# Kernel tuning notes

Measured on AMD Instinct MI355X. Metric: run time of the kernel, lower is better.

## Reference

```python
import jax, jax.numpy as jnp
import numpy as np

N_DRUG, N_MICROBE = 1500, 1572
N = N_DRUG + N_MICROBE          # 3072 nodes
F_IN = 1546                     # raw feature dim (fc1: 1546 -> 256)
D0 = 256                        # GCN input dim after fc1
H1 = H2 = 128                   # GCN hidden dims (H1 + H2 = 256)
B = 16384                       # number of (left,right) query pairs


def _sym_norm(A):
    # D^{-1/2} A D^{-1/2} (no self loops), zeros kept for isolated nodes
    deg = A.sum(axis=1)
    d = jnp.where(deg > 0, jax.lax.rsqrt(deg), 0.0)
    return A * d[:, None] * d[None, :]


def _compute_inf(adj, L):
    # dl.compute_inf: L-hop influence = L-th power of sym-normalized adjacency
    An = _sym_norm(adj)
    M = An
    for _ in range(L - 1):
        M = M @ An
    return M


def _gcn_norm(W):
    # GCNConv normalization: add self loops (weight 1), sym-normalize by weighted degree
    Ahat = W + jnp.eye(W.shape[0], dtype=W.dtype)
    deg = Ahat.sum(axis=1)
    d = jnp.where(deg > 0, jax.lax.rsqrt(deg), 0.0)
    return Ahat * d[:, None] * d[None, :]


def _glorot(key, shape):
    return jax.random.normal(key, shape, dtype=jnp.float32) / np.sqrt(shape[0])


def setup_inputs() -> dict:
    key = jax.random.key(0)
    ks = jax.random.split(key, 24)
    u = jax.random.uniform(ks[0], (N, N), dtype=jnp.float32)
    w = jax.random.uniform(ks[1], (N, N), dtype=jnp.float32)
    adj = jnp.where(u < 0.01, w, 0.0)
    adj = jnp.maximum(adj, adj.T)
    X = jax.random.normal(ks[2], (N, F_IN), dtype=jnp.float32)
    left = jax.random.randint(ks[3], (B,), 0, N)
    right = jax.random.randint(ks[4], (B,), 0, N)
    return dict(
        left=left, right=right, X=X, adj=adj, threshold=jnp.float32(1e-4),
        W_fc1=_glorot(ks[5], (F_IN, D0)), b_fc1=jnp.zeros((D0,), jnp.float32),
        Wg1=_glorot(ks[6], (D0, H1)), bg1=jnp.zeros((H1,), jnp.float32),
        Wg2=_glorot(ks[7], (H1, H2)), bg2=jnp.zeros((H2,), jnp.float32),
        Wg3=_glorot(ks[8], (D0, H1)), bg3=jnp.zeros((H1,), jnp.float32),
        Wg4=_glorot(ks[9], (H1, H2)), bg4=jnp.zeros((H2,), jnp.float32),
        Wg5=_glorot(ks[10], (D0, H1)), bg5=jnp.zeros((H1,), jnp.float32),
        Wg6=_glorot(ks[11], (H1, H2)), bg6=jnp.zeros((H2,), jnp.float32),
        cnn_k=jax.random.normal(ks[12], (1, 3, 3, 3), dtype=jnp.float32) * 0.1,
        cnn_b=jnp.zeros((1,), jnp.float32),
        W_a=_glorot(ks[13], (2 * (H1 + H2), 64)), b_a=jnp.zeros((64,), jnp.float32),
        W_b=_glorot(ks[14], (64, 2)), b_b=jnp.zeros((2,), jnp.float32),
    )


def reference(left, right, X, adj, threshold,
              W_fc1, b_fc1, Wg1, bg1, Wg2, bg2, Wg3, bg3, Wg4, bg4,
              Wg5, bg5, Wg6, bg6, cnn_k, cnn_b, W_a, b_a, W_b, b_b):
    X0 = jax.nn.relu(X @ W_fc1 + b_fc1)  # fc1: [N, 1546] -> [N, 256]

    def branch(mask_src, Wa, ba, Wb, bb):
        # dynamically thresholded edges carry the ORIGINAL adj weights
        Wadj = jnp.where(mask_src > threshold, adj, 0.0)
        An = _gcn_norm(Wadj)                       # [N, N]
        e1 = jax.nn.relu(An @ (X0 @ Wa) + ba)      # GCNConv 1
        e2 = jax.nn.relu(An @ (e1 @ Wb) + bb)      # GCNConv 2
        return jnp.concatenate([e1, e2], axis=1)   # [N, 256]

    emb_l2 = branch(_compute_inf(adj, 2), Wg1, bg1, Wg2, bg2)
    emb_l1 = branch(_compute_inf(adj, 1), Wg3, bg3, Wg4, bg4)
    emb_l0 = branch(adj, Wg5, bg5, Wg6, bg6)

    emb = jnp.stack([emb_l0, emb_l1, emb_l2], axis=0)[None]  # [1, 3, N, 256]
    conv = jax.lax.conv_general_dilated(
        emb, cnn_k, window_strides=(1, 1), padding=[(2, 2), (2, 2)],
        rhs_dilation=(2, 2), dimension_numbers=('NCHW', 'OIHW', 'NCHW'))
    emb_all = conv[0, 0] + cnn_b[0]                # [N, 256]

    pair = jnp.concatenate([emb_all[left], emb_all[right]], axis=1)  # [B, 512]
    h = jax.nn.relu(pair @ W_a + b_a)              # dropout is identity at eval
    logits = h @ W_b + b_b                         # [B, 2]
    return logits, emb_all
```

## Files before the change

### kernel.cpp

```cpp
#include <hip/hip_runtime.h>

#define NN 3072
#define FIN 1546
#define KP 1568
#define MAXR 192

#define XS4_BLOCKS (NN * KP / 1024)
#define WSPLIT_BLOCKS (256 * KP / 256)
#define WGA_BLOCKS 384
#define CSR_BLOCKS (NN / 4)
#define FC1_BLOCKS (NN / 16 * 4)

typedef __attribute__((ext_vector_type(8))) __bf16 bf16x8;
typedef __attribute__((ext_vector_type(4))) __bf16 bf16x4;
typedef __attribute__((ext_vector_type(4))) float f32x4;

__global__ __launch_bounds__(256) void prep1_k(const float* __restrict__ X,
                                               __bf16* __restrict__ Xh, __bf16* __restrict__ Xl,
                                               const float* __restrict__ W,
                                               __bf16* __restrict__ WhT, __bf16* __restrict__ WlT,
                                               const float* __restrict__ Wga0,
                                               const float* __restrict__ Wga1,
                                               const float* __restrict__ Wga2,
                                               __bf16* __restrict__ WgaTh, __bf16* __restrict__ WgaTl) {
    int bid = blockIdx.x;
    if (bid < XS4_BLOCKS) {
        int e = (bid * 256 + threadIdx.x) * 4;
        int i = e / KP, c = e - i * KP;
        const float* xr = X + (size_t)i * FIN + c;
        float x0 = (c + 0 < FIN) ? xr[0] : 0.f;
        float x1 = (c + 1 < FIN) ? xr[1] : 0.f;
        float x2 = (c + 2 < FIN) ? xr[2] : 0.f;
        float x3 = (c + 3 < FIN) ? xr[3] : 0.f;
        __bf16 h0 = (__bf16)x0, h1 = (__bf16)x1, h2 = (__bf16)x2, h3 = (__bf16)x3;
        bf16x4 hv = {h0, h1, h2, h3};
        bf16x4 lv = {(__bf16)(x0 - (float)h0), (__bf16)(x1 - (float)h1),
                     (__bf16)(x2 - (float)h2), (__bf16)(x3 - (float)h3)};
        *(bf16x4*)(Xh + e) = hv;
        *(bf16x4*)(Xl + e) = lv;
        return;
    }
    bid -= XS4_BLOCKS;
    if (bid < WSPLIT_BLOCKS) {
        int idx = bid * 256 + threadIdx.x;
        int c = idx / KP, k = idx - c * KP;
        float x = (k < FIN) ? W[(size_t)k * 256 + c] : 0.f;
        __bf16 h = (__bf16)x;
        WhT[idx] = h;
        WlT[idx] = (__bf16)(x - (float)h);
        return;
    }
    bid -= WSPLIT_BLOCKS;
    int idx = bid * 256 + threadIdx.x;
    int b = idx >> 15, r = idx & 32767;
    int c = r >> 8, k = r & 255;
    const float* Wp = (b == 0) ? Wga0 : (b == 1) ? Wga1 : Wga2;
    float x = Wp[k * 128 + c];
    __bf16 h = (__bf16)x;
    WgaTh[idx] = h;
    WgaTl[idx] = (__bf16)(x - (float)h);
}

__global__ __launch_bounds__(256) void fc1csr_k(const float* __restrict__ adj,
                                                int* __restrict__ cols, float* __restrict__ vals,
                                                int* __restrict__ cnt, float* __restrict__ dvec,
                                                const __bf16* __restrict__ Xh,
                                                const __bf16* __restrict__ Xl,
                                                const __bf16* __restrict__ WhT,
                                                const __bf16* __restrict__ WlT,
                                                const float* __restrict__ bias,
                                                __bf16* __restrict__ X0h,
                                                __bf16* __restrict__ X0l) {
    int bid = blockIdx.x, tid = threadIdx.x;
    if (bid < FC1_BLOCKS) {
        int rt = bid >> 2;
        int c0 = (bid & 3) * 64;
        int w = tid >> 6, lane = tid & 63;
        int m = lane & 15, q = lane >> 4;
        int r0 = rt * 16;
        int cw = c0 + w * 16;
        const __bf16* xh = Xh + (size_t)(r0 + m) * KP + q * 8;
        const __bf16* xl = Xl + (size_t)(r0 + m) * KP + q * 8;
        const __bf16* bh = WhT + (size_t)(cw + m) * KP + q * 8;
        const __bf16* bl = WlT + (size_t)(cw + m) * KP + q * 8;

        f32x4 acc;
        #pragma unroll
        for (int r = 0; r < 4; r++) acc[r] = 0.f;

        #pragma unroll 7
        for (int ks = 0; ks < KP; ks += 32) {
            bf16x8 ah = *(const bf16x8*)(xh + ks);
            bf16x8 al = *(const bf16x8*)(xl + ks);
            bf16x8 bhv = *(const bf16x8*)(bh + ks);
            bf16x8 blv = *(const bf16x8*)(bl + ks);
            acc = __builtin_amdgcn_mfma_f32_16x16x32_bf16(ah, bhv, acc, 0, 0, 0);
            acc = __builtin_amdgcn_mfma_f32_16x16x32_bf16(ah, blv, acc, 0, 0, 0);
            acc = __builtin_amdgcn_mfma_f32_16x16x32_bf16(al, bhv, acc, 0, 0, 0);
        }
        int col = cw + m;
        float bv = bias[col];
        #pragma unroll
        for (int r = 0; r < 4; r++) {
            int row = r0 + q * 4 + r;
            float s = fmaxf(acc[r] + bv, 0.f);
            __bf16 h = (__bf16)s;
            X0h[(size_t)row * 256 + col] = h;
            X0l[(size_t)row * 256 + col] = (__bf16)(s - (float)h);
        }
        return;
    }
    int i = (bid - FC1_BLOCKS) * 4 + (tid >> 6);
    int lane = tid & 63;
    const float* row = adj + (size_t)i * NN;
    unsigned long long below = (1ull << lane) - 1ull;
    float s = 0.f; int count = 0;
    int base = i * MAXR;
    for (int c0 = 0; c0 < NN; c0 += 256) {
        float4 a4 = *(const float4*)(row + c0 + lane * 4);
        float a[4] = {a4.x, a4.y, a4.z, a4.w};
        s += a[0] + a[1] + a[2] + a[3];
        unsigned long long bal[4];
        #pragma unroll
        for (int u = 0; u < 4; u++) bal[u] = __ballot(a[u] != 0.f);
        int before = 0;
        #pragma unroll
        for (int u = 0; u < 4; u++) before += __popcll(bal[u] & below);
        int local = 0;
        #pragma unroll
        for (int u = 0; u < 4; u++) {
            if (a[u] != 0.f) {
                int pos = count + before + local;
                if (pos < MAXR) { cols[base + pos] = c0 + lane * 4 + u; vals[base + pos] = a[u]; }
                local++;
            }
        }
        int tot = 0;
        #pragma unroll
        for (int u = 0; u < 4; u++) tot += __popcll(bal[u]);
        count += tot;
    }
    for (int off = 32; off; off >>= 1) s += __shfl_xor(s, off);
    if (lane == 0) {
        cnt[i] = count < MAXR ? count : MAXR;
        dvec[i] = (s > 0.f) ? 1.0f / sqrtf(s) : 0.f;
    }
}

__global__ __launch_bounds__(256) void maskg1_k(const int* __restrict__ cols,
                                                const float* __restrict__ vals,
                                                const int* __restrict__ cnt,
                                                const float* __restrict__ dvec,
                                                const float* __restrict__ thrp,
                                                int* __restrict__ mcols,
                                                float* __restrict__ mvals,
                                                int* __restrict__ mcnt,
                                                float* __restrict__ db,
                                                const __bf16* __restrict__ X0h,
                                                const __bf16* __restrict__ X0l,
                                                const __bf16* __restrict__ WgaTh,
                                                const __bf16* __restrict__ WgaTl,
                                                float* __restrict__ XWall) {
    __shared__ float ds[NN];
    __shared__ int lcols[MAXR];
    __shared__ float lvals[MAXR];
    __shared__ int lcnt;
    __shared__ float osum;
    int bid = blockIdx.x, tid = threadIdx.x;

    if (bid >= 3 * NN) {
        int g = bid - 3 * NN;
        int bx = g % 48, by = (g / 48) & 1, bz = g / 96;
        int w = tid >> 6, lane = tid & 63;
        int m = lane & 15, q = lane >> 4;
        int i0 = bx * 64, c0 = by * 64;
        int rowA = i0 + w * 16 + m;
        const __bf16* ah = X0h + (size_t)rowA * 256 + q * 8;
        const __bf16* al = X0l + (size_t)rowA * 256 + q * 8;
        const __bf16* bh0 = WgaTh + (size_t)bz * 128 * 256 + (size_t)(c0 + m) * 256 + q * 8;
        const __bf16* bl0 = WgaTl + (size_t)bz * 128 * 256 + (size_t)(c0 + m) * 256 + q * 8;

        f32x4 acc[4];
        #pragma unroll
        for (int ct = 0; ct < 4; ct++)
            #pragma unroll
            for (int r = 0; r < 4; r++) acc[ct][r] = 0.f;

        for (int ks = 0; ks < 256; ks += 32) {
            bf16x8 a_h = *(const bf16x8*)(ah + ks);
            bf16x8 a_l = *(const bf16x8*)(al + ks);
            #pragma unroll
            for (int ct = 0; ct < 4; ct++) {
                bf16x8 b_h = *(const bf16x8*)(bh0 + (size_t)ct * 16 * 256 + ks);
                bf16x8 b_l = *(const bf16x8*)(bl0 + (size_t)ct * 16 * 256 + ks);
                acc[ct] = __builtin_amdgcn_mfma_f32_16x16x32_bf16(a_h, b_h, acc[ct], 0, 0, 0);
                acc[ct] = __builtin_amdgcn_mfma_f32_16x16x32_bf16(a_h, b_l, acc[ct], 0, 0, 0);
                acc[ct] = __builtin_amdgcn_mfma_f32_16x16x32_bf16(a_l, b_h, acc[ct], 0, 0, 0);
            }
        }
        float* outp = XWall + (size_t)bz * NN * 128;
        int rowBase = i0 + w * 16 + q * 4;
        #pragma unroll
        for (int ct = 0; ct < 4; ct++) {
            int col = c0 + ct * 16 + m;
            #pragma unroll
            for (int r = 0; r < 4; r++)
                outp[(size_t)(rowBase + r) * 128 + col] = acc[ct][r];
        }
        return;
    }

    int t = bid;
    int mode, i;
    if (t < NN)          { mode = 2; i = t; }
    else if (t < 2 * NN) { mode = 0; i = t - NN; }
    else                 { mode = 1; i = t - 2 * NN; }

    mcols += (size_t)mode * NN * MAXR;
    mvals += (size_t)mode * NN * MAXR;
    mcnt  += (size_t)mode * NN;
    db    += (size_t)mode * NN;
    int ni = cnt[i], base = i * MAXR;
    float thr = *thrp;
    float di = dvec[i];

    if (mode < 2) {
        if (tid == 0) lcnt = 0;
        __syncthreads();
        float s = 0.f;
        if (tid < ni) {
            int j = cols[base + tid];
            float a = vals[base + tid];
            float m = (mode == 0) ? a : a * di * dvec[j];
            if (m > thr) {
                int p = atomicAdd(&lcnt, 1);
                mcols[base + p] = j;
                mvals[base + p] = a;
                s = a;
            }
        }
        ds[tid] = s; __syncthreads();
        for (int off = 128; off; off >>= 1) {
            if (tid < off) ds[tid] += ds[tid + off];
            __syncthreads();
        }
        if (tid == 0) {
            mcnt[i] = lcnt;
            db[i] = 1.0f / sqrtf(ds[0] + 1.0f);
        }
        return;
    }

    if (tid == 0) { osum = 0.f; lcnt = 0; }
    for (int j = tid; j < NN; j += 256) ds[j] = 0.f;
    __syncthreads();
    for (int t2 = tid; t2 < ni; t2 += 256) {
        int j = cols[base + t2];
        float a = vals[base + t2];
        lcols[t2] = j; lvals[t2] = a;
        ds[j] = a * dvec[j] * dvec[j];
    }
    __syncthreads();
    int lane = tid & 63, wv = tid >> 6;
    int sub = lane & 7, dg = lane >> 3;
    for (int o = wv * 8 + dg; o < ni; o += 32) {
        int j = lcols[o];
        int nj = cnt[j], bj = j * MAXR;
        float dot = 0.f;
        for (int t2 = sub; t2 < nj; t2 += 8)
            dot += vals[bj + t2] * ds[cols[bj + t2]];
        #pragma unroll
        for (int off = 4; off; off >>= 1) dot += __shfl_xor(dot, off);
        if (sub == 0 && di * dvec[j] * dot > thr) {
            int p = atomicAdd(&lcnt, 1);
            mcols[base + p] = j;
            mvals[base + p] = lvals[o];
            atomicAdd(&osum, lvals[o]);
        }
    }
    __syncthreads();
    if (tid == 0) {
        mcnt[i] = lcnt;
        db[i] = 1.0f / sqrtf(osum + 1.0f);
    }
}

__global__ __launch_bounds__(256) void spmm3_k(const int* __restrict__ mcols,
                                               const float* __restrict__ mvals,
                                               const int* __restrict__ mcnt,
                                               const float* __restrict__ db,
                                               const float* __restrict__ Xin,
                                               const float* __restrict__ bias0,
                                               const float* __restrict__ bias1,
                                               const float* __restrict__ bias2,
                                               float* __restrict__ embf, int coff,
                                               const float* __restrict__ Wgb0,
                                               const float* __restrict__ Wgb1,
                                               const float* __restrict__ Wgb2,
                                               float* __restrict__ HW2out) {
    __shared__ float lcoef[MAXR];
    __shared__ int lj[MAXR];
    __shared__ float4 part[8][32];
    __shared__ float e1row[128];
    __shared__ float part2[2][128];
    int i = blockIdx.x, tid = threadIdx.x, b = blockIdx.y;
    mcols += (size_t)b * NN * MAXR;
    mvals += (size_t)b * NN * MAXR;
    mcnt  += (size_t)b * NN;
    db    += (size_t)b * NN;
    const float* Xb = Xin + (size_t)b * NN * 128;
    const float* bias = (b == 0) ? bias0 : (b == 1) ? bias1 : bias2;
    float dbi = db[i];
    int n = mcnt[i], base = i * MAXR;
    if (tid < n) {
        int j = mcols[base + tid];
        lj[tid] = j;
        lcoef[tid] = mvals[base + tid] * dbi * db[j];
    }
    __syncthreads();
    int g = tid >> 5, c4 = (tid & 31) << 2;
    float4 acc = make_float4(0.f, 0.f, 0.f, 0.f);
    float4 acc2 = make_float4(0.f, 0.f, 0.f, 0.f);
    if (g == 0) {
        float4 x = *(const float4*)&Xb[(size_t)i * 128 + c4];
        float d2 = dbi * dbi;
        acc = make_float4(d2 * x.x, d2 * x.y, d2 * x.z, d2 * x.w);
    }
    int t = g;
    for (; t + 8 < n; t += 16) {
        float cf0 = lcoef[t];
        float4 x0 = *(const float4*)&Xb[(size_t)lj[t] * 128 + c4];
        float cf1 = lcoef[t + 8];
        float4 x1 = *(const float4*)&Xb[(size_t)lj[t + 8] * 128 + c4];
        acc.x += cf0 * x0.x; acc.y += cf0 * x0.y; acc.z += cf0 * x0.z; acc.w += cf0 * x0.w;
        acc2.x += cf1 * x1.x; acc2.y += cf1 * x1.y; acc2.z += cf1 * x1.z; acc2.w += cf1 * x1.w;
    }
    if (t < n) {
        float cf = lcoef[t];
        float4 x = *(const float4*)&Xb[(size_t)lj[t] * 128 + c4];
        acc.x += cf * x.x; acc.y += cf * x.y; acc.z += cf * x.z; acc.w += cf * x.w;
    }
    acc.x += acc2.x; acc.y += acc2.y; acc.z += acc2.z; acc.w += acc2.w;
    part[g][tid & 31] = acc;
    __syncthreads();
    if (tid < 32) {
        float4 s = part[0][tid];
        #pragma unroll
        for (int gg = 1; gg < 8; gg++) {
            float4 t4 = part[gg][tid];
            s.x += t4.x; s.y += t4.y; s.z += t4.z; s.w += t4.w;
        }
        int cc = tid << 2;
        float4 bv = *(const float4*)&bias[cc];
        s.x = fmaxf(s.x + bv.x, 0.f); s.y = fmaxf(s.y + bv.y, 0.f);
        s.z = fmaxf(s.z + bv.z, 0.f); s.w = fmaxf(s.w + bv.w, 0.f);
        *(float4*)&embf[((size_t)b * NN + i) * 256 + coff + cc] = s;
        *(float4*)&e1row[cc] = s;
    }
    if (!HW2out) return;
    __syncthreads();
    int o = tid & 127, h = tid >> 7;
    const float* Wg = (b == 0) ? Wgb0 : (b == 1) ? Wgb1 : Wgb2;
    float ha = 0.f;
    int kbase = h * 64;
    const float* wp = Wg + (size_t)kbase * 128 + o;
    #pragma unroll 8
    for (int kk = 0; kk < 64; kk++)
        ha += e1row[kbase + kk] * wp[(size_t)kk * 128];
    part2[h][o] = ha;
    __syncthreads();
    if (tid < 128)
        HW2out[((size_t)b * NN + i) * 128 + tid] = part2[0][tid] + part2[1][tid];
}

__global__ __launch_bounds__(256) void convuv_k(const float* __restrict__ emb,
                                                const float* __restrict__ ck,
                                                const float* __restrict__ cb,
                                                float* __restrict__ outf,
                                                const float* __restrict__ Wa,
                                                float* __restrict__ uvp) {
    __shared__ float rows[3][3][256];
    __shared__ float embrow[256];
    __shared__ float part2[2][128];
    int n = blockIdx.x, c = threadIdx.x;
    #pragma unroll
    for (int i = 0; i < 3; i++)
        #pragma unroll
        for (int kh = 0; kh < 3; kh++) {
            int nn2 = n + 2 * kh - 2;
            rows[i][kh][c] = (nn2 >= 0 && nn2 < NN) ? emb[((size_t)i * NN + nn2) * 256 + c] : 0.f;
        }
    __syncthreads();
    float s = cb[0];
    #pragma unroll
    for (int i = 0; i < 3; i++)
        #pragma unroll
        for (int kh = 0; kh < 3; kh++)
            #pragma unroll
            for (int kw = 0; kw < 3; kw++) {
                int cc = c + 2 * kw - 2;
                if (cc >= 0 && cc < 256)
                    s += rows[i][kh][cc] * ck[(i * 3 + kh) * 3 + kw];
            }
    size_t idx = (size_t)n * 256 + c;
    outf[idx] = s;
    embrow[c] = s;
    __syncthreads();
    int o = c & 127, h = c >> 7;
    int kbase = h * 128;
    const float* wp = (o < 64) ? (Wa + (size_t)kbase * 64 + o)
                               : (Wa + (size_t)(256 + kbase) * 64 + (o - 64));
    float acc = 0.f;
    #pragma unroll 8
    for (int kk = 0; kk < 128; kk++)
        acc += embrow[kbase + kk] * wp[(size_t)kk * 64];
    part2[h][o] = acc;
    __syncthreads();
    if (c < 128)
        uvp[(size_t)n * 128 + c] = part2[0][c] + part2[1][c];
}

__global__ __launch_bounds__(256) void pairuv_k(const int* __restrict__ left,
                                                const int* __restrict__ right,
                                                const float* __restrict__ uvp,
                                                const float* __restrict__ ba,
                                                const float* __restrict__ Wb,
                                                const float* __restrict__ bb,
                                                float* __restrict__ out) {
    int tid = threadIdx.x;
    int w = tid >> 6, c = tid & 63;
    int base = blockIdx.x * 16 + w * 4;
    float bac = ba[c];
    float w0 = Wb[c * 2], w1 = Wb[c * 2 + 1];
    float b0 = bb[0], b1 = bb[1];
    #pragma unroll
    for (int pp = 0; pp < 4; pp++) {
        int row = base + pp;
        int l = left[row], r = right[row];
        float h = uvp[(size_t)l * 128 + c] + uvp[(size_t)r * 128 + 64 + c] + bac;
        h = fmaxf(h, 0.f);
        float s0 = h * w0, s1 = h * w1;
        for (int off = 32; off; off >>= 1) {
            s0 += __shfl_xor(s0, off);
            s1 += __shfl_xor(s1, off);
        }
        if (c == 0) {
            out[row * 2]     = s0 + b0;
            out[row * 2 + 1] = s1 + b1;
        }
    }
}

extern "C" void kernel_launch(void* const* d_in, const int* in_sizes, int n_in,
                              void* d_out, int out_size, void* d_ws, size_t ws_size,
                              hipStream_t stream) {
    const int* left  = (const int*)d_in[0];
    const int* right = (const int*)d_in[1];
    const float* X    = (const float*)d_in[2];
    const float* adj  = (const float*)d_in[3];
    const float* thr  = (const float*)d_in[4];
    const float* Wfc1 = (const float*)d_in[5];
    const float* bfc1 = (const float*)d_in[6];
    const float* Wga[3] = { (const float*)d_in[15], (const float*)d_in[11], (const float*)d_in[7] };
    const float* bga[3] = { (const float*)d_in[16], (const float*)d_in[12], (const float*)d_in[8] };
    const float* Wgb[3] = { (const float*)d_in[17], (const float*)d_in[13], (const float*)d_in[9] };
    const float* bgb[3] = { (const float*)d_in[18], (const float*)d_in[14], (const float*)d_in[10] };
    const float* cnnk = (const float*)d_in[19];
    const float* cnnb = (const float*)d_in[20];
    const float* Wa_  = (const float*)d_in[21];
    const float* ba_  = (const float*)d_in[22];
    const float* Wb_  = (const float*)d_in[23];
    const float* bb_  = (const float*)d_in[24];

    char* p = (char*)d_ws;
    auto take = [&](size_t n) { char* q = p; p += (n + 255) & ~(size_t)255; return q; };
    float* dvec = (float*)take(NN * 4);
    float* db3  = (float*)take((size_t)3 * NN * 4);
    int*   cnt  = (int*)take(NN * 4);
    int*   mcnt3 = (int*)take((size_t)3 * NN * 4);
    int*   cols = (int*)take((size_t)NN * MAXR * 4);
    float* vals = (float*)take((size_t)NN * MAXR * 4);
    int*   mcols3 = (int*)take((size_t)3 * NN * MAXR * 4);
    float* mvals3 = (float*)take((size_t)3 * NN * MAXR * 4);
    __bf16* X0h  = (__bf16*)take((size_t)NN * 256 * 2);
    __bf16* X0l  = (__bf16*)take((size_t)NN * 256 * 2);
    float* XWall = (float*)take((size_t)3 * NN * 128 * 4);
    float* HW2all= (float*)take((size_t)3 * NN * 128 * 4);
    float* embf  = (float*)take((size_t)3 * NN * 256 * 4);
    __bf16* Xh   = (__bf16*)take((size_t)NN * KP * 2);
    __bf16* Xl   = (__bf16*)take((size_t)NN * KP * 2);
    __bf16* WhT  = (__bf16*)take((size_t)256 * KP * 2);
    __bf16* WlT  = (__bf16*)take((size_t)256 * KP * 2);
    __bf16* WgaTh = (__bf16*)take((size_t)3 * 128 * 256 * 2);
    __bf16* WgaTl = (__bf16*)take((size_t)3 * 128 * 256 * 2);
    float* uvp   = (float*)take((size_t)NN * 128 * 4);

    float* out_logits = (float*)d_out;
    float* out_emb = out_logits + 32768;

    prep1_k<<<XS4_BLOCKS + WSPLIT_BLOCKS + WGA_BLOCKS, 256, 0, stream>>>(
        X, Xh, Xl, Wfc1, WhT, WlT, Wga[0], Wga[1], Wga[2], WgaTh, WgaTl);

    fc1csr_k<<<FC1_BLOCKS + CSR_BLOCKS, 256, 0, stream>>>(
        adj, cols, vals, cnt, dvec, Xh, Xl, WhT, WlT, bfc1, X0h, X0l);

    maskg1_k<<<3 * NN + 288, 256, 0, stream>>>(cols, vals, cnt, dvec, thr,
                                               mcols3, mvals3, mcnt3, db3,
                                               X0h, X0l, WgaTh, WgaTl, XWall);

    spmm3_k<<<dim3(NN, 3), 256, 0, stream>>>(mcols3, mvals3, mcnt3, db3, XWall,
                                             bga[0], bga[1], bga[2], embf, 0,
                                             Wgb[0], Wgb[1], Wgb[2], HW2all);

    spmm3_k<<<dim3(NN, 3), 256, 0, stream>>>(mcols3, mvals3, mcnt3, db3, HW2all,
                                             bgb[0], bgb[1], bgb[2], embf, 128,
                                             (const float*)0, (const float*)0, (const float*)0,
                                             (float*)0);

    convuv_k<<<NN, 256, 0, stream>>>(embf, cnnk, cnnb, out_emb, Wa_, uvp);

    pairuv_k<<<16384 / 16, 256, 0, stream>>>(left, right, uvp, ba_, Wb_, bb_, out_logits);
}
```

Before: 322.9 us.

## Split-K fc1 GEMM with on-the-fly bf16 splitting and reshuffled kernel stages

Drops the separate pass that pre-split X into bf16 hi/lo buffers. The fc1 GEMM now reads fp32 X directly, splits it in registers, and runs as a 7-way split-K over 64x64 tiles, writing partial sums that a new reduction kernel adds up with bias and ReLU. The CSR build moves into the prep kernel with a software-prefetched row load. The mask stages are regrouped so the cheap modes run beside the GEMM and the L2 mask runs beside the reduction, and the Wga GEMM gets its own kernel. This trades the X conversion traffic and a poorly parallelised fc1 for extra partial-sum traffic (7xNx256 fp32) and one more launch.

```diff
diff --git a/kernel.cpp b/kernel.cpp
--- a/kernel.cpp
+++ b/kernel.cpp
@@ -4,43 +4,29 @@
 #define FIN 1546
 #define KP 1568
 #define MAXR 192
-
-#define XS4_BLOCKS (NN * KP / 1024)
+#define KSPLIT 7
+#define KSLICE 224
+
 #define WSPLIT_BLOCKS (256 * KP / 256)
 #define WGA_BLOCKS 384
 #define CSR_BLOCKS (NN / 4)
-#define FC1_BLOCKS (NN / 16 * 4)
+#define FC1_BLOCKS (48 * 4 * KSPLIT)
+#define RED_BLOCKS 768
 
 typedef __attribute__((ext_vector_type(8))) __bf16 bf16x8;
 typedef __attribute__((ext_vector_type(4))) __bf16 bf16x4;
 typedef __attribute__((ext_vector_type(4))) float f32x4;
 
-__global__ __launch_bounds__(256) void prep1_k(const float* __restrict__ X,
-                                               __bf16* __restrict__ Xh, __bf16* __restrict__ Xl,
-                                               const float* __restrict__ W,
-                                               __bf16* __restrict__ WhT, __bf16* __restrict__ WlT,
-                                               const float* __restrict__ Wga0,
-                                               const float* __restrict__ Wga1,
-                                               const float* __restrict__ Wga2,
-                                               __bf16* __restrict__ WgaTh, __bf16* __restrict__ WgaTl) {
+__global__ __launch_bounds__(256) void prep_k(const float* __restrict__ adj,
+                                              int* __restrict__ cols, float* __restrict__ vals,
+                                              int* __restrict__ cnt, float* __restrict__ dvec,
+                                              const float* __restrict__ W,
+                                              __bf16* __restrict__ WhT, __bf16* __restrict__ WlT,
+                                              const float* __restrict__ Wga0,
+                                              const float* __restrict__ Wga1,
+                                              const float* __restrict__ Wga2,
+                                              __bf16* __restrict__ WgaTh, __bf16* __restrict__ WgaTl) {
     int bid = blockIdx.x;
-    if (bid < XS4_BLOCKS) {
-        int e = (bid * 256 + threadIdx.x) * 4;
-        int i = e / KP, c = e - i * KP;
-        const float* xr = X + (size_t)i * FIN + c;
-        float x0 = (c + 0 < FIN) ? xr[0] : 0.f;
-        float x1 = (c + 1 < FIN) ? xr[1] : 0.f;
-        float x2 = (c + 2 < FIN) ? xr[2] : 0.f;
-        float x3 = (c + 3 < FIN) ? xr[3] : 0.f;
-        __bf16 h0 = (__bf16)x0, h1 = (__bf16)x1, h2 = (__bf16)x2, h3 = (__bf16)x3;
-        bf16x4 hv = {h0, h1, h2, h3};
-        bf16x4 lv = {(__bf16)(x0 - (float)h0), (__bf16)(x1 - (float)h1),
-                     (__bf16)(x2 - (float)h2), (__bf16)(x3 - (float)h3)};
-        *(bf16x4*)(Xh + e) = hv;
-        *(bf16x4*)(Xl + e) = lv;
-        return;
-    }
-    bid -= XS4_BLOCKS;
     if (bid < WSPLIT_BLOCKS) {
         int idx = bid * 256 + threadIdx.x;
         int c = idx / KP, k = idx - c * KP;
@@ -51,73 +37,28 @@
         return;
     }
     bid -= WSPLIT_BLOCKS;
-    int idx = bid * 256 + threadIdx.x;
-    int b = idx >> 15, r = idx & 32767;
-    int c = r >> 8, k = r & 255;
-    const float* Wp = (b == 0) ? Wga0 : (b == 1) ? Wga1 : Wga2;
-    float x = Wp[k * 128 + c];
-    __bf16 h = (__bf16)x;
-    WgaTh[idx] = h;
-    WgaTl[idx] = (__bf16)(x - (float)h);
-}
-
-__global__ __launch_bounds__(256) void fc1csr_k(const float* __restrict__ adj,
-                                                int* __restrict__ cols, float* __restrict__ vals,
-                                                int* __restrict__ cnt, float* __restrict__ dvec,
-                                                const __bf16* __restrict__ Xh,
-                                                const __bf16* __restrict__ Xl,
-                                                const __bf16* __restrict__ WhT,
-                                                const __bf16* __restrict__ WlT,
-                                                const float* __restrict__ bias,
-                                                __bf16* __restrict__ X0h,
-                                                __bf16* __restrict__ X0l) {
-    int bid = blockIdx.x, tid = threadIdx.x;
-    if (bid < FC1_BLOCKS) {
-        int rt = bid >> 2;
-        int c0 = (bid & 3) * 64;
-        int w = tid >> 6, lane = tid & 63;
-        int m = lane & 15, q = lane >> 4;
-        int r0 = rt * 16;
-        int cw = c0 + w * 16;
-        const __bf16* xh = Xh + (size_t)(r0 + m) * KP + q * 8;
-        const __bf16* xl = Xl + (size_t)(r0 + m) * KP + q * 8;
-        const __bf16* bh = WhT + (size_t)(cw + m) * KP + q * 8;
-        const __bf16* bl = WlT + (size_t)(cw + m) * KP + q * 8;
-
-        f32x4 acc;
-        #pragma unroll
-        for (int r = 0; r < 4; r++) acc[r] = 0.f;
-
-        #pragma unroll 7
-        for (int ks = 0; ks < KP; ks += 32) {
-            bf16x8 ah = *(const bf16x8*)(xh + ks);
-            bf16x8 al = *(const bf16x8*)(xl + ks);
-            bf16x8 bhv = *(const bf16x8*)(bh + ks);
-            bf16x8 blv = *(const bf16x8*)(bl + ks);
-            acc = __builtin_amdgcn_mfma_f32_16x16x32_bf16(ah, bhv, acc, 0, 0, 0);
-            acc = __builtin_amdgcn_mfma_f32_16x16x32_bf16(ah, blv, acc, 0, 0, 0);
-            acc = __builtin_amdgcn_mfma_f32_16x16x32_bf16(al, bhv, acc, 0, 0, 0);
-        }
-        int col = cw + m;
-        float bv = bias[col];
-        #pragma unroll
-        for (int r = 0; r < 4; r++) {
-            int row = r0 + q * 4 + r;
-            float s = fmaxf(acc[r] + bv, 0.f);
-            __bf16 h = (__bf16)s;
-            X0h[(size_t)row * 256 + col] = h;
-            X0l[(size_t)row * 256 + col] = (__bf16)(s - (float)h);
-        }
+    if (bid < WGA_BLOCKS) {
+        int idx = bid * 256 + threadIdx.x;
+        int b = idx >> 15, r = idx & 32767;
+        int c = r >> 8, k = r & 255;
+        const float* Wp = (b == 0) ? Wga0 : (b == 1) ? Wga1 : Wga2;
+        float x = Wp[k * 128 + c];
+        __bf16 h = (__bf16)x;
+        WgaTh[idx] = h;
+        WgaTl[idx] = (__bf16)(x - (float)h);
         return;
     }
-    int i = (bid - FC1_BLOCKS) * 4 + (tid >> 6);
-    int lane = tid & 63;
+    bid -= WGA_BLOCKS;
+    int i = bid * 4 + (threadIdx.x >> 6);
+    int lane = threadIdx.x & 63;
     const float* row = adj + (size_t)i * NN;
     unsigned long long below = (1ull << lane) - 1ull;
     float s = 0.f; int count = 0;
     int base = i * MAXR;
+    float4 a4 = *(const float4*)(row + lane * 4);
     for (int c0 = 0; c0 < NN; c0 += 256) {
-        float4 a4 = *(const float4*)(row + c0 + lane * 4);
+        float4 nxt;
+        if (c0 + 256 < NN) nxt = *(const float4*)(row + c0 + 256 + lane * 4);
         float a[4] = {a4.x, a4.y, a4.z, a4.w};
         s += a[0] + a[1] + a[2] + a[3];
         unsigned long long bal[4];
@@ -139,6 +80,7 @@
         #pragma unroll
         for (int u = 0; u < 4; u++) tot += __popcll(bal[u]);
         count += tot;
+        a4 = nxt;
     }
     for (int off = 32; off; off >>= 1) s += __shfl_xor(s, off);
     if (lane == 0) {
@@ -147,38 +89,35 @@
     }
 }
 
-__global__ __launch_bounds__(256) void maskg1_k(const int* __restrict__ cols,
-                                                const float* __restrict__ vals,
-                                                const int* __restrict__ cnt,
-                                                const float* __restrict__ dvec,
-                                                const float* __restrict__ thrp,
-                                                int* __restrict__ mcols,
-                                                float* __restrict__ mvals,
-                                                int* __restrict__ mcnt,
-                                                float* __restrict__ db,
-                                                const __bf16* __restrict__ X0h,
-                                                const __bf16* __restrict__ X0l,
-                                                const __bf16* __restrict__ WgaTh,
-                                                const __bf16* __restrict__ WgaTl,
-                                                float* __restrict__ XWall) {
-    __shared__ float ds[NN];
-    __shared__ int lcols[MAXR];
-    __shared__ float lvals[MAXR];
+__global__ __launch_bounds__(256) void fc1mask01_k(const float* __restrict__ X,
+                                                   const __bf16* __restrict__ WhT,
+                                                   const __bf16* __restrict__ WlT,
+                                                   float* __restrict__ Cpart,
+                                                   const int* __restrict__ cols,
+                                                   const float* __restrict__ vals,
+                                                   const int* __restrict__ cnt,
+                                                   const float* __restrict__ dvec,
+                                                   const float* __restrict__ thrp,
+                                                   int* __restrict__ mcols,
+                                                   float* __restrict__ mvals,
+                                                   int* __restrict__ mcnt,
+                                                   float* __restrict__ db) {
+    __shared__ float ds[256];
     __shared__ int lcnt;
-    __shared__ float osum;
     int bid = blockIdx.x, tid = threadIdx.x;
 
-    if (bid >= 3 * NN) {
-        int g = bid - 3 * NN;
-        int bx = g % 48, by = (g / 48) & 1, bz = g / 96;
+    if (bid < FC1_BLOCKS) {
+        int bx = bid % 48;
+        int byz = bid / 48;
+        int by = byz % 4, z = byz / 4;
         int w = tid >> 6, lane = tid & 63;
         int m = lane & 15, q = lane >> 4;
         int i0 = bx * 64, c0 = by * 64;
+        int k0 = z * KSLICE;
         int rowA = i0 + w * 16 + m;
-        const __bf16* ah = X0h + (size_t)rowA * 256 + q * 8;
-        const __bf16* al = X0l + (size_t)rowA * 256 + q * 8;
-        const __bf16* bh0 = WgaTh + (size_t)bz * 128 * 256 + (size_t)(c0 + m) * 256 + q * 8;
-        const __bf16* bl0 = WgaTl + (size_t)bz * 128 * 256 + (size_t)(c0 + m) * 256 + q * 8;
+        const float* xrow = X + (size_t)rowA * FIN + k0 + q * 8;
+        const __bf16* bh0 = WhT + (size_t)(c0 + m) * KP + k0 + q * 8;
+        const __bf16* bl0 = WlT + (size_t)(c0 + m) * KP + k0 + q * 8;
 
         f32x4 acc[4];
         #pragma unroll
@@ -186,35 +125,51 @@
             #pragma unroll
             for (int r = 0; r < 4; r++) acc[ct][r] = 0.f;
 
-        for (int ks = 0; ks < 256; ks += 32) {
-            bf16x8 a_h = *(const bf16x8*)(ah + ks);
-            bf16x8 a_l = *(const bf16x8*)(al + ks);
+        #pragma unroll 2
+        for (int ks = 0; ks < KSLICE; ks += 32) {
+            float xv[8];
+            if (z < KSPLIT - 1) {
+                const float2* xp = (const float2*)(xrow + ks);
+                float2 p0 = xp[0], p1 = xp[1], p2 = xp[2], p3 = xp[3];
+                xv[0] = p0.x; xv[1] = p0.y; xv[2] = p1.x; xv[3] = p1.y;
+                xv[4] = p2.x; xv[5] = p2.y; xv[6] = p3.x; xv[7] = p3.y;
+            } else {
+                int kb = k0 + q * 8 + ks;
+                #pragma unroll
+                for (int e = 0; e < 8; e++)
+                    xv[e] = (kb + e < FIN) ? xrow[ks + e] : 0.f;
+            }
+            bf16x8 ah, al;
+            #pragma unroll
+            for (int e = 0; e < 8; e++) {
+                __bf16 h = (__bf16)xv[e];
+                ah[e] = h;
+                al[e] = (__bf16)(xv[e] - (float)h);
+            }
             #pragma unroll
             for (int ct = 0; ct < 4; ct++) {
-                bf16x8 b_h = *(const bf16x8*)(bh0 + (size_t)ct * 16 * 256 + ks);
-                bf16x8 b_l = *(const bf16x8*)(bl0 + (size_t)ct * 16 * 256 + ks);
-                acc[ct] = __builtin_amdgcn_mfma_f32_16x16x32_bf16(a_h, b_h, acc[ct], 0, 0, 0);
-                acc[ct] = __builtin_amdgcn_mfma_f32_16x16x32_bf16(a_h, b_l, acc[ct], 0, 0, 0);
-                acc[ct] = __builtin_amdgcn_mfma_f32_16x16x32_bf16(a_l, b_h, acc[ct], 0, 0, 0);
+                bf16x8 bh = *(const bf16x8*)(bh0 + (size_t)ct * 16 * KP + ks);
+                bf16x8 bl = *(const bf16x8*)(bl0 + (size_t)ct * 16 * KP + ks);
+                acc[ct] = __builtin_amdgcn_mfma_f32_16x16x32_bf16(ah, bh, acc[ct], 0, 0, 0);
+                acc[ct] = __builtin_amdgcn_mfma_f32_16x16x32_bf16(ah, bl, acc[ct], 0, 0, 0);
+                acc[ct] = __builtin_amdgcn_mfma_f32_16x16x32_bf16(al, bh, acc[ct], 0, 0, 0);
             }
         }
-        float* outp = XWall + (size_t)bz * NN * 128;
+        float* outp = Cpart + (size_t)z * NN * 256;
         int rowBase = i0 + w * 16 + q * 4;
         #pragma unroll
         for (int ct = 0; ct < 4; ct++) {
             int col = c0 + ct * 16 + m;
             #pragma unroll
             for (int r = 0; r < 4; r++)
-                outp[(size_t)(rowBase + r) * 128 + col] = acc[ct][r];
+                outp[(size_t)(rowBase + r) * 256 + col] = acc[ct][r];
         }
         return;
     }
 
-    int t = bid;
-    int mode, i;
-    if (t < NN)          { mode = 2; i = t; }
-    else if (t < 2 * NN) { mode = 0; i = t - NN; }
-    else                 { mode = 1; i = t - 2 * NN; }
+    int t = bid - FC1_BLOCKS;
+    int mode = (t < NN) ? 0 : 1;
+    int i = (t < NN) ? t : t - NN;
 
     mcols += (size_t)mode * NN * MAXR;
     mvals += (size_t)mode * NN * MAXR;
@@ -224,32 +179,80 @@
     float thr = *thrp;
     float di = dvec[i];
 
-    if (mode < 2) {
-        if (tid == 0) lcnt = 0;
+    if (tid == 0) lcnt = 0;
+    __syncthreads();
+    float s = 0.f;
+    if (tid < ni) {
+        int j = cols[base + tid];
+        float a = vals[base + tid];
+        float mv = (mode == 0) ? a : a * di * dvec[j];
+        if (mv > thr) {
+            int p = atomicAdd(&lcnt, 1);
+            mcols[base + p] = j;
+            mvals[base + p] = a;
+            s = a;
+        }
+    }
+    ds[tid] = s; __syncthreads();
+    for (int off = 128; off; off >>= 1) {
+        if (tid < off) ds[tid] += ds[tid + off];
         __syncthreads();
-        float s = 0.f;
-        if (tid < ni) {
-            int j = cols[base + tid];
-            float a = vals[base + tid];
-            float m = (mode == 0) ? a : a * di * dvec[j];
-            if (m > thr) {
-                int p = atomicAdd(&lcnt, 1);
-                mcols[base + p] = j;
-                mvals[base + p] = a;
-                s = a;
-            }
-        }
-        ds[tid] = s; __syncthreads();
-        for (int off = 128; off; off >>= 1) {
-            if (tid < off) ds[tid] += ds[tid + off];
-            __syncthreads();
-        }
-        if (tid == 0) {
-            mcnt[i] = lcnt;
-            db[i] = 1.0f / sqrtf(ds[0] + 1.0f);
-        }
+    }
+    if (tid == 0) {
+        mcnt[i] = lcnt;
+        db[i] = 1.0f / sqrtf(ds[0] + 1.0f);
+    }
+}
+
+__global__ __launch_bounds__(256) void redm2_k(const float* __restrict__ Cpart,
+                                               const float* __restrict__ bias,
+                                               __bf16* __restrict__ X0h,
+                                               __bf16* __restrict__ X0l,
+                                               const int* __restrict__ cols,
+                                               const float* __restrict__ vals,
+                                               const int* __restrict__ cnt,
+                                               const float* __restrict__ dvec,
+                                               const float* __restrict__ thrp,
+                                               int* __restrict__ mcols,
+                                               float* __restrict__ mvals,
+                                               int* __restrict__ mcnt,
+                                               float* __restrict__ db) {
+    __shared__ float ds[NN];
+    __shared__ int lcols[MAXR];
+    __shared__ float lvals[MAXR];
+    __shared__ int lcnt;
+    __shared__ float osum;
+    int bid = blockIdx.x, tid = threadIdx.x;
+
+    if (bid < RED_BLOCKS) {
+        int idx4 = bid * 256 + tid;
+        int i = idx4 >> 6, c4 = (idx4 & 63) << 2;
+        float4 s = ((const float4*)Cpart)[idx4];
+        #pragma unroll
+        for (int z = 1; z < KSPLIT; z++) {
+            float4 t4 = ((const float4*)(Cpart + (size_t)z * NN * 256))[idx4];
+            s.x += t4.x; s.y += t4.y; s.z += t4.z; s.w += t4.w;
+        }
+        float4 b = *(const float4*)&bias[c4];
+        s.x = fmaxf(s.x + b.x, 0.f); s.y = fmaxf(s.y + b.y, 0.f);
+        s.z = fmaxf(s.z + b.z, 0.f); s.w = fmaxf(s.w + b.w, 0.f);
+        __bf16 h0 = (__bf16)s.x, h1 = (__bf16)s.y, h2 = (__bf16)s.z, h3 = (__bf16)s.w;
+        bf16x4 hv = {h0, h1, h2, h3};
+        bf16x4 lv = {(__bf16)(s.x - (float)h0), (__bf16)(s.y - (float)h1),
+                     (__bf16)(s.z - (float)h2), (__bf16)(s.w - (float)h3)};
+        *(bf16x4*)(X0h + (size_t)i * 256 + c4) = hv;
+        *(bf16x4*)(X0l + (size_t)i * 256 + c4) = lv;
         return;
     }
+
+    int i = bid - RED_BLOCKS;
+    mcols += (size_t)2 * NN * MAXR;
+    mvals += (size_t)2 * NN * MAXR;
+    mcnt  += (size_t)2 * NN;
+    db    += (size_t)2 * NN;
+    int ni = cnt[i], base = i * MAXR;
+    float thr = *thrp;
+    float di = dvec[i];
 
     if (tid == 0) { osum = 0.f; lcnt = 0; }
     for (int j = tid; j < NN; j += 256) ds[j] = 0.f;
@@ -282,6 +285,51 @@
     if (tid == 0) {
         mcnt[i] = lcnt;
         db[i] = 1.0f / sqrtf(osum + 1.0f);
+    }
+}
+
+__global__ __launch_bounds__(256) void gemm1_k(const __bf16* __restrict__ X0h,
+                                               const __bf16* __restrict__ X0l,
+                                               const __bf16* __restrict__ WgaTh,
+                                               const __bf16* __restrict__ WgaTl,
+                                               float* __restrict__ XWall) {
+    int tid = threadIdx.x;
+    int w = tid >> 6, lane = tid & 63;
+    int m = lane & 15, q = lane >> 4;
+    int i0 = blockIdx.x * 64, c0 = blockIdx.y * 64;
+    int bz = blockIdx.z;
+    int rowA = i0 + w * 16 + m;
+    const __bf16* ah = X0h + (size_t)rowA * 256 + q * 8;
+    const __bf16* al = X0l + (size_t)rowA * 256 + q * 8;
+    const __bf16* bh0 = WgaTh + (size_t)bz * 128 * 256 + (size_t)(c0 + m) * 256 + q * 8;
+    const __bf16* bl0 = WgaTl + (size_t)bz * 128 * 256 + (size_t)(c0 + m) * 256 + q * 8;
+
+    f32x4 acc[4];
+    #pragma unroll
+    for (int ct = 0; ct < 4; ct++)
+        #pragma unroll
+        for (int r = 0; r < 4; r++) acc[ct][r] = 0.f;
+
+    for (int ks = 0; ks < 256; ks += 32) {
+        bf16x8 a_h = *(const bf16x8*)(ah + ks);
+        bf16x8 a_l = *(const bf16x8*)(al + ks);
+        #pragma unroll
+        for (int ct = 0; ct < 4; ct++) {
+            bf16x8 b_h = *(const bf16x8*)(bh0 + (size_t)ct * 16 * 256 + ks);
+            bf16x8 b_l = *(const bf16x8*)(bl0 + (size_t)ct * 16 * 256 + ks);
+            acc[ct] = __builtin_amdgcn_mfma_f32_16x16x32_bf16(a_h, b_h, acc[ct], 0, 0, 0);
+            acc[ct] = __builtin_amdgcn_mfma_f32_16x16x32_bf16(a_h, b_l, acc[ct], 0, 0, 0);
+            acc[ct] = __builtin_amdgcn_mfma_f32_16x16x32_bf16(a_l, b_h, acc[ct], 0, 0, 0);
+        }
+    }
+    float* outp = XWall + (size_t)bz * NN * 128;
+    int rowBase = i0 + w * 16 + q * 4;
+    #pragma unroll
+    for (int ct = 0; ct < 4; ct++) {
+        int col = c0 + ct * 16 + m;
+        #pragma unroll
+        for (int r = 0; r < 4; r++)
+            outp[(size_t)(rowBase + r) * 128 + col] = acc[ct][r];
     }
 }
 
@@ -482,13 +530,12 @@
     float* vals = (float*)take((size_t)NN * MAXR * 4);
     int*   mcols3 = (int*)take((size_t)3 * NN * MAXR * 4);
     float* mvals3 = (float*)take((size_t)3 * NN * MAXR * 4);
+    float* Cpart = (float*)take((size_t)KSPLIT * NN * 256 * 4);
     __bf16* X0h  = (__bf16*)take((size_t)NN * 256 * 2);
     __bf16* X0l  = (__bf16*)take((size_t)NN * 256 * 2);
     float* XWall = (float*)take((size_t)3 * NN * 128 * 4);
     float* HW2all= (float*)take((size_t)3 * NN * 128 * 4);
     float* embf  = (float*)take((size_t)3 * NN * 256 * 4);
-    __bf16* Xh   = (__bf16*)take((size_t)NN * KP * 2);
-    __bf16* Xl   = (__bf16*)take((size_t)NN * KP * 2);
     __bf16* WhT  = (__bf16*)take((size_t)256 * KP * 2);
     __bf16* WlT  = (__bf16*)take((size_t)256 * KP * 2);
     __bf16* WgaTh = (__bf16*)take((size_t)3 * 128 * 256 * 2);
@@ -498,15 +545,19 @@
     float* out_logits = (float*)d_out;
     float* out_emb = out_logits + 32768;
 
-    prep1_k<<<XS4_BLOCKS + WSPLIT_BLOCKS + WGA_BLOCKS, 256, 0, stream>>>(
-        X, Xh, Xl, Wfc1, WhT, WlT, Wga[0], Wga[1], Wga[2], WgaTh, WgaTl);
-
-    fc1csr_k<<<FC1_BLOCKS + CSR_BLOCKS, 256, 0, stream>>>(
-        adj, cols, vals, cnt, dvec, Xh, Xl, WhT, WlT, bfc1, X0h, X0l);
-
-    maskg1_k<<<3 * NN + 288, 256, 0, stream>>>(cols, vals, cnt, dvec, thr,
-                                               mcols3, mvals3, mcnt3, db3,
-                                               X0h, X0l, WgaTh, WgaTl, XWall);
+    prep_k<<<WSPLIT_BLOCKS + WGA_BLOCKS + CSR_BLOCKS, 256, 0, stream>>>(
+        adj, cols, vals, cnt, dvec, Wfc1, WhT, WlT,
+        Wga[0], Wga[1], Wga[2], WgaTh, WgaTl);
+
+    fc1mask01_k<<<FC1_BLOCKS + 2 * NN, 256, 0, stream>>>(
+        X, WhT, WlT, Cpart,
+        cols, vals, cnt, dvec, thr, mcols3, mvals3, mcnt3, db3);
+
+    redm2_k<<<RED_BLOCKS + NN, 256, 0, stream>>>(
+        Cpart, bfc1, X0h, X0l,
+        cols, vals, cnt, dvec, thr, mcols3, mvals3, mcnt3, db3);
+
+    gemm1_k<<<dim3(NN / 64, 2, 3), 256, 0, stream>>>(X0h, X0l, WgaTh, WgaTl, XWall);
 
     spmm3_k<<<dim3(NN, 3), 256, 0, stream>>>(mcols3, mvals3, mcnt3, db3, XWall,
                                              bga[0], bga[1], bga[2], embf, 0,
```

Result: faster. 305.4 us (-5.4%).
